# Optimization experiments

Measured on AMD Instinct MI355X. Metric: run time of the kernel, lower is better.

## Reference

```python
import jax, jax.numpy as jnp
import numpy as np

# Fixed problem sizes (equal-sized batch segments, matching setup_inputs)
B, N, M = 4, 4096, 16384          # clouds, coarse pts/cloud, fine pts/cloud
C_IN, C_SKIP, K = 256, 256, 3     # feature dims, knn k
CH = [C_IN + C_SKIP, 512, 256]    # MLP channels
EPS = 1e-16


def setup_inputs() -> dict:
    key = jax.random.key(0)
    ks = jax.random.split(key, 6)
    x = jax.random.normal(ks[0], (B * N, C_IN), jnp.float32)
    pos = jax.random.uniform(ks[1], (B * N, 3), jnp.float32)
    batch = jnp.repeat(jnp.arange(B, dtype=jnp.int64), N)
    x_skip = jax.random.normal(ks[2], (B * M, C_SKIP), jnp.float32)
    pos_skip = jax.random.uniform(ks[3], (B * M, 3), jnp.float32)
    batch_skip = jnp.repeat(jnp.arange(B, dtype=jnp.int64), M)
    W1 = jax.random.normal(ks[4], (CH[0], CH[1]), jnp.float32) / np.sqrt(CH[0]).astype(np.float32)
    b1 = jnp.zeros((CH[1],), jnp.float32)
    W2 = jax.random.normal(ks[5], (CH[1], CH[2]), jnp.float32) / np.sqrt(CH[1]).astype(np.float32)
    b2 = jnp.zeros((CH[2],), jnp.float32)
    return dict(x=x, pos=pos, batch=batch, x_skip=x_skip, pos_skip=pos_skip,
                batch_skip=batch_skip, W1=W1, b1=b1, W2=W2, b2=b2)


def _knn_interpolate(x, pos, pos_skip):
    """torch_geometric.nn.knn_interpolate with equal-sized batch segments."""
    xb = x.reshape(B, N, C_IN)
    ps = pos.reshape(B, N, 3)
    qs = pos_skip.reshape(B, M, 3)
    # squared pairwise distances [B, M, N]
    d2 = (jnp.sum(qs * qs, -1)[:, :, None]
          - 2.0 * jnp.einsum('bmd,bnd->bmn', qs, ps)
          + jnp.sum(ps * ps, -1)[:, None, :])
    neg_d2, idx = jax.lax.top_k(-d2, K)                # k smallest distances, [B,M,K]
    w = 1.0 / jnp.clip(-neg_d2, EPS)                   # inverse squared distance weights
    feats = jax.vmap(lambda f, i: f[i])(xb, idx)       # gather: [B, M, K, C_IN]
    y = jnp.sum(w[..., None] * feats, axis=2) / jnp.sum(w, axis=2)[..., None]
    return y.reshape(B * M, C_IN)


def reference(x, pos, batch, x_skip, pos_skip, batch_skip, W1, b1, W2, b2):
    y = _knn_interpolate(x, pos, pos_skip)
    h = jnp.concatenate([y, x_skip], axis=1)           # [B*M, 512]
    h = jax.nn.relu(h @ W1 + b1)
    h = jax.nn.relu(h @ W2 + b2)
    return h, pos_skip, batch_skip
```

## Files before the change

### kernel.cpp

```cpp
#include <hip/hip_runtime.h>
#include <stdint.h>

#define NB 4
#define NPTS 4096
#define MPTS 16384
#define CIN 256
#define CH0 512
#define CH1 512
#define CH2 256
#define ROWS (NB * MPTS)
#define POS_OUT_OFF (ROWS * CH2)
#define BATCH_OUT_OFF (POS_OUT_OFF + ROWS * 3)
#define CELL_CAP 40
#define QCAP 96

using u16 = unsigned short;
using u32 = unsigned int;
using u64 = unsigned long long;

typedef __bf16 bf16x8 __attribute__((ext_vector_type(8)));
typedef float f32x4 __attribute__((ext_vector_type(4)));

__device__ __forceinline__ u16 f2bf(float f) {
  u32 u = __builtin_bit_cast(u32, f);
  u32 r = u + 0x7fffu + ((u >> 16) & 1u);
  return (u16)(r >> 16);
}

__device__ __forceinline__ u32 flipf(float f) {
  u32 u = __builtin_bit_cast(u32, f);
  return u ^ ((u32)((int)u >> 31) | 0x80000000u);
}
__device__ __forceinline__ float unflipf(u32 f) {
  u32 m = (~(u32)((int)f >> 31)) | 0x80000000u;
  return __builtin_bit_cast(float, f ^ m);
}

__device__ __forceinline__ void ins3(u64 v, u64& k0, u64& k1, u64& k2) {
  u64 a = k0 < v ? v : k0;
  k0 = k0 < v ? k0 : v;
  u64 bb = k1 < a ? a : k1;
  k1 = k1 < a ? k1 : a;
  k2 = k2 < bb ? k2 : bb;
}

__device__ __forceinline__ void merge3(u64 r0, u64 r1, u64 r2,
                                       u64& k0, u64& k1, u64& k2) {
  u64 t = k0 < r0 ? r0 : k0;
  k0 = k0 < r0 ? k0 : r0;
  u64 u = k1 < r1 ? k1 : r1;
  u64 mtu = t < u ? u : t;
  k1 = t < u ? t : u;
  u64 v = k2 < r2 ? k2 : r2;
  k2 = mtu < v ? mtu : v;
}

__device__ __forceinline__ u64 shfl_xor_u64_w8(u64 v, int mask) {
  u32 lo = (u32)v, hi = (u32)(v >> 32);
  lo = (u32)__shfl_xor((int)lo, mask, 8);
  hi = (u32)__shfl_xor((int)hi, mask, 8);
  return ((u64)hi << 32) | lo;
}

__global__ __launch_bounds__(256) void prep_kernel(
    const float* __restrict__ W1, const float* __restrict__ W2,
    u16* __restrict__ W1s, u16* __restrict__ W2s) {
  const int t = blockIdx.x * 256 + threadIdx.x;
  if (t < 32768) {
    const int l = t & 63, ni = (t >> 6) & 3, wd = (t >> 8) & 7, kt = t >> 11;
    const int fr = l & 15, g = l >> 4;
    const int n = wd * 64 + ni * 16 + fr;
    u16 o[8];
#pragma unroll
    for (int j = 0; j < 8; ++j)
      o[j] = f2bf(W1[(kt * 32 + g * 8 + j) * CH1 + n]);
    *(uint4*)(W1s + (size_t)t * 8) = *(const uint4*)o;
  } else {
    const int c = t - 32768;
    const int l = c & 63, ni = (c >> 6) & 1, wd = (c >> 7) & 7, kt = c >> 10;
    const int fr = l & 15, g = l >> 4;
    const int n = wd * 32 + ni * 16 + fr;
    u16 o[8];
#pragma unroll
    for (int j = 0; j < 8; ++j)
      o[j] = f2bf(W2[(kt * 32 + g * 8 + j) * CH2 + n]);
    *(uint4*)(W2s + (size_t)c * 8) = *(const uint4*)o;
  }
}

__global__ __launch_bounds__(256) void tail_kernel(
    const float* __restrict__ pos_skip, const int* __restrict__ batch_skip,
    float* __restrict__ out) {
  int t = blockIdx.x * 256 + threadIdx.x;
  if (t < ROWS * 3) {
    out[POS_OUT_OFF + t] = pos_skip[t];
  } else {
    int u = t - ROWS * 3;
    out[BATCH_OUT_OFF + u] = (float)batch_skip[u];
  }
}

__global__ __launch_bounds__(256) void build_kernel(
    const float* __restrict__ pos, float4* __restrict__ pts4,
    u32* __restrict__ cellCnt, int* __restrict__ cellIdx) {
#pragma clang fp contract(off)
  const int i = blockIdx.x * 256 + threadIdx.x;
  const float x = pos[i * 3 + 0], y = pos[i * 3 + 1], z = pos[i * 3 + 2];
  pts4[i] = make_float4(x, y, z, (x * x + y * y) + z * z);
  const int b = i >> 12;
  int cx = (int)(x * 8.0f); cx = cx < 0 ? 0 : (cx > 7 ? 7 : cx);
  int cy = (int)(y * 8.0f); cy = cy < 0 ? 0 : (cy > 7 ? 7 : cy);
  int cz = (int)(z * 8.0f); cz = cz < 0 ? 0 : (cz > 7 ? 7 : cz);
  const int c = b * 512 + cz * 64 + cy * 8 + cx;
  const u32 slot = atomicAdd(&cellCnt[c], 1u);
  if (slot < CELL_CAP) cellIdx[c * CELL_CAP + slot] = i;
}

__global__ __launch_bounds__(256) void qbin_kernel(
    const float* __restrict__ pos_skip, u32* __restrict__ qCnt,
    int* __restrict__ qIdx) {
  const int q = blockIdx.x * 256 + threadIdx.x;
  const int b = q >> 14;
  const float qx = pos_skip[q * 3 + 0];
  const float qy = pos_skip[q * 3 + 1];
  const float qz = pos_skip[q * 3 + 2];
  int cx = (int)(qx * 8.0f); cx = cx < 0 ? 0 : (cx > 7 ? 7 : cx);
  int cy = (int)(qy * 8.0f); cy = cy < 0 ? 0 : (cy > 7 ? 7 : cy);
  int cz = (int)(qz * 8.0f); cz = cz < 0 ? 0 : (cz > 7 ? 7 : cz);
  const int c = b * 512 + cz * 64 + cy * 8 + cx;
  const u32 slot = atomicAdd(&qCnt[c], 1u);
  if (slot < QCAP) qIdx[c * QCAP + slot] = q;
}

__global__ __launch_bounds__(256) void knn_kernel(
    const float4* __restrict__ pts4, const u32* __restrict__ cellCnt,
    const int* __restrict__ cellIdx, const u32* __restrict__ qCnt,
    const int* __restrict__ qIdx, const float* __restrict__ pos_skip,
    int* __restrict__ idx_out, float* __restrict__ w_out) {
#pragma clang fp contract(off)
  __shared__ float4 scand[27 * CELL_CAP];
  __shared__ int    scgi[27 * CELL_CAP];
  __shared__ u32    scnt[27];
  __shared__ int    sbase[27];
  __shared__ u32    nCand;
  const int tid = threadIdx.x;
  const int b = blockIdx.x >> 9;
  const int cell = blockIdx.x & 511;
  const int cz = cell >> 6, cy = (cell >> 3) & 7, cx = cell & 7;
  const int x0 = cx > 0 ? cx - 1 : 0, x1 = cx < 7 ? cx + 1 : 7;
  const int y0 = cy > 0 ? cy - 1 : 0, y1 = cy < 7 ? cy + 1 : 7;
  const int z0 = cz > 0 ? cz - 1 : 0, z1 = cz < 7 ? cz + 1 : 7;
  const int nx = x1 - x0 + 1, ny = y1 - y0 + 1, nz = z1 - z0 + 1;
  const int ncells = nx * ny * nz;
  if (tid == 0) nCand = 0;
  if (tid < ncells) {
    const int lz = tid / (nx * ny);
    const int rem = tid - lz * nx * ny;
    const int ly = rem / nx;
    const int lx = rem - ly * nx;
    const int cg = b * 512 + (z0 + lz) * 64 + (y0 + ly) * 8 + (x0 + lx);
    u32 cnt = cellCnt[cg];
    scnt[tid] = cnt > CELL_CAP ? CELL_CAP : cnt;
    sbase[tid] = cg * CELL_CAP;
  }
  __syncthreads();
  const int slots = ncells * CELL_CAP;
  for (int s = tid; s < slots; s += 256) {
    const int ci = s / CELL_CAP;
    const int sl = s - ci * CELL_CAP;
    if ((u32)sl < scnt[ci]) {
      const int gi = cellIdx[sbase[ci] + sl];
      const float4 p = pts4[gi];
      const u32 d = atomicAdd(&nCand, 1u);
      scand[d] = p;
      scgi[d] = gi;
    }
  }
  __syncthreads();
  const int nC = (int)nCand;
  u32 nq = qCnt[b * 512 + cell];
  if (nq > QCAP) nq = QCAP;
  const int qbase = (b * 512 + cell) * QCAP;
  const int g = tid >> 3;
  const int sub = tid & 7;

  for (int r0q = 0; r0q < (int)nq; r0q += 32) {
    const int qslot = r0q + g;
    if (qslot < (int)nq) {
      const int q = qIdx[qbase + qslot];
      const float qx = pos_skip[q * 3 + 0];
      const float qy = pos_skip[q * 3 + 1];
      const float qz = pos_skip[q * 3 + 2];
      const float q2 = (qx * qx + qy * qy) + qz * qz;
      u64 k0 = ~0ull, k1 = ~0ull, k2 = ~0ull;
      for (int s = sub; s < nC; s += 8) {
        const float4 p = scand[s];
        const float dot = fmaf(qz, p.z, fmaf(qy, p.y, qx * p.x));
        const float tv = (q2 - 2.0f * dot) + p.w;
        const u64 key = ((u64)flipf(tv) << 32) | (u32)scgi[s];
        ins3(key, k0, k1, k2);
      }
#pragma unroll
      for (int mask = 1; mask < 8; mask <<= 1) {
        const u64 r0 = shfl_xor_u64_w8(k0, mask);
        const u64 r1 = shfl_xor_u64_w8(k1, mask);
        const u64 r2 = shfl_xor_u64_w8(k2, mask);
        merge3(r0, r1, r2, k0, k1, k2);
      }
      float m2tv = unflipf((u32)(k2 >> 32));
      if (!(m2tv <= 0.015625f - 1e-5f)) {
        k0 = k1 = k2 = ~0ull;
        const int ex0 = cx > 1 ? cx - 2 : 0, ex1 = cx < 6 ? cx + 2 : 7;
        const int ey0 = cy > 1 ? cy - 2 : 0, ey1 = cy < 6 ? cy + 2 : 7;
        const int ez0 = cz > 1 ? cz - 2 : 0, ez1 = cz < 6 ? cz + 2 : 7;
        for (int zz = ez0; zz <= ez1; ++zz)
          for (int yy = ey0; yy <= ey1; ++yy)
            for (int xx = ex0; xx <= ex1; ++xx) {
              const int cg = b * 512 + zz * 64 + yy * 8 + xx;
              u32 cnt = cellCnt[cg];
              if (cnt > CELL_CAP) cnt = CELL_CAP;
              const int cb = cg * CELL_CAP;
              for (int s = sub; s < (int)cnt; s += 8) {
                const int gi = cellIdx[cb + s];
                const float4 p = pts4[gi];
                const float dot = fmaf(qz, p.z, fmaf(qy, p.y, qx * p.x));
                const float tv = (q2 - 2.0f * dot) + p.w;
                ins3(((u64)flipf(tv) << 32) | (u32)gi, k0, k1, k2);
              }
            }
#pragma unroll
        for (int mask = 1; mask < 8; mask <<= 1) {
          const u64 r0 = shfl_xor_u64_w8(k0, mask);
          const u64 r1 = shfl_xor_u64_w8(k1, mask);
          const u64 r2 = shfl_xor_u64_w8(k2, mask);
          merge3(r0, r1, r2, k0, k1, k2);
        }
        m2tv = unflipf((u32)(k2 >> 32));
        if (!(m2tv <= 0.0625f - 1e-5f)) {
          k0 = k1 = k2 = ~0ull;
          const int base = b * NPTS;
          for (int i = sub; i < NPTS; i += 8) {
            const int gi = base + i;
            const float4 p = pts4[gi];
            const float dot = fmaf(qz, p.z, fmaf(qy, p.y, qx * p.x));
            const float tv = (q2 - 2.0f * dot) + p.w;
            ins3(((u64)flipf(tv) << 32) | (u32)gi, k0, k1, k2);
          }
#pragma unroll
          for (int mask = 1; mask < 8; mask <<= 1) {
            const u64 r0 = shfl_xor_u64_w8(k0, mask);
            const u64 r1 = shfl_xor_u64_w8(k1, mask);
            const u64 r2 = shfl_xor_u64_w8(k2, mask);
            merge3(r0, r1, r2, k0, k1, k2);
          }
        }
      }
      if (sub == 0) {
        const float t0 = unflipf((u32)(k0 >> 32));
        const float t1 = unflipf((u32)(k1 >> 32));
        const float t2 = unflipf((u32)(k2 >> 32));
        const float w0 = 1.0f / fmaxf(t0, 1e-16f);
        const float w1 = 1.0f / fmaxf(t1, 1e-16f);
        const float w2 = 1.0f / fmaxf(t2, 1e-16f);
        const float wsum = (w0 + w1) + w2;
        const float inv = 1.0f / wsum;
        idx_out[q * 3 + 0] = (int)(u32)k0;
        idx_out[q * 3 + 1] = (int)(u32)k1;
        idx_out[q * 3 + 2] = (int)(u32)k2;
        w_out[q * 3 + 0] = w0 * inv;
        w_out[q * 3 + 1] = w1 * inv;
        w_out[q * 3 + 2] = w2 * inv;
      }
    }
  }
}

__global__ __launch_bounds__(512, 2) void fused_mlp_kernel(
    const float* __restrict__ x, const int* __restrict__ idx,
    const float* __restrict__ w, const float* __restrict__ x_skip,
    const u16* __restrict__ W1s, const float* __restrict__ b1,
    const u16* __restrict__ W2s, const float* __restrict__ b2,
    float* __restrict__ out) {
  __shared__ __align__(16) u16 Abuf[64 * 512];
  const int tid = threadIdx.x;
  const int m0 = blockIdx.x * 64;

  {
    const int row = tid >> 3;
    const int sub = tid & 7;
    const int gr = m0 + row;
    u16* rowp = Abuf + row * 512;
    const int rx = row & 7;
    if (sub < 4) {
      const int i0 = idx[gr * 3 + 0], i1 = idx[gr * 3 + 1], i2 = idx[gr * 3 + 2];
      const float w0 = w[gr * 3 + 0], w1 = w[gr * 3 + 1], w2 = w[gr * 3 + 2];
      const float4* p0 = (const float4*)(x + (size_t)i0 * CIN + sub * 64);
      const float4* p1 = (const float4*)(x + (size_t)i1 * CIN + sub * 64);
      const float4* p2 = (const float4*)(x + (size_t)i2 * CIN + sub * 64);
#pragma unroll
      for (int c = 0; c < 8; ++c) {
        const float4 a0 = p0[c * 2], a1 = p1[c * 2], a2 = p2[c * 2];
        const float4 d0 = p0[c * 2 + 1], d1 = p1[c * 2 + 1], d2 = p2[c * 2 + 1];
        u16 o[8];
        o[0] = f2bf(fmaf(w0, a0.x, fmaf(w1, a1.x, w2 * a2.x)));
        o[1] = f2bf(fmaf(w0, a0.y, fmaf(w1, a1.y, w2 * a2.y)));
        o[2] = f2bf(fmaf(w0, a0.z, fmaf(w1, a1.z, w2 * a2.z)));
        o[3] = f2bf(fmaf(w0, a0.w, fmaf(w1, a1.w, w2 * a2.w)));
        o[4] = f2bf(fmaf(w0, d0.x, fmaf(w1, d1.x, w2 * d2.x)));
        o[5] = f2bf(fmaf(w0, d0.y, fmaf(w1, d1.y, w2 * d2.y)));
        o[6] = f2bf(fmaf(w0, d0.z, fmaf(w1, d1.z, w2 * d2.z)));
        o[7] = f2bf(fmaf(w0, d0.w, fmaf(w1, d1.w, w2 * d2.w)));
        const int vg = sub * 8 + c;
        *(uint4*)(rowp + (vg ^ rx) * 8) = *(const uint4*)o;
      }
    } else {
      const float4* ps = (const float4*)(x_skip + (size_t)gr * CIN + (sub - 4) * 64);
#pragma unroll
      for (int c = 0; c < 8; ++c) {
        const float4 a = ps[c * 2], d = ps[c * 2 + 1];
        u16 o[8];
        o[0] = f2bf(a.x); o[1] = f2bf(a.y); o[2] = f2bf(a.z); o[3] = f2bf(a.w);
        o[4] = f2bf(d.x); o[5] = f2bf(d.y); o[6] = f2bf(d.z); o[7] = f2bf(d.w);
        const int vg = 32 + (sub - 4) * 8 + c;
        *(uint4*)(rowp + (vg ^ rx) * 8) = *(const uint4*)o;
      }
    }
  }
  __syncthreads();

  const int wid = tid >> 6;
  const int lane = tid & 63;
  const int fr = lane & 15;
  const int g = lane >> 4;
  const int frx = fr & 7;

  f32x4 acc[4][4];
#pragma unroll
  for (int mi = 0; mi < 4; mi++)
#pragma unroll
    for (int ni = 0; ni < 4; ni++) acc[mi][ni] = (f32x4){0.f, 0.f, 0.f, 0.f};

  {
    const u16* B1 = W1s + wid * 2048 + lane * 8;
    bf16x8 bf[2][4];
#pragma unroll
    for (int ni = 0; ni < 4; ni++)
      bf[0][ni] = *(const bf16x8*)(B1 + ni * 512);
    for (int kt = 0; kt < 16; ++kt) {
      const int cur = kt & 1;
      if (kt < 15) {
        const u16* nb = B1 + (kt + 1) * 16384;
#pragma unroll
        for (int ni = 0; ni < 4; ni++)
          bf[cur ^ 1][ni] = *(const bf16x8*)(nb + ni * 512);
      }
      bf16x8 af[4];
#pragma unroll
      for (int mi = 0; mi < 4; mi++)
        af[mi] = *(const bf16x8*)&Abuf[(mi * 16 + fr) * 512 +
                                       (((kt * 4 + g) ^ frx) * 8)];
#pragma unroll
      for (int mi = 0; mi < 4; mi++)
#pragma unroll
        for (int ni = 0; ni < 4; ni++)
          acc[mi][ni] = __builtin_amdgcn_mfma_f32_16x16x32_bf16(
              af[mi], bf[cur][ni], acc[mi][ni], 0, 0, 0);
    }
  }
  __syncthreads();

  {
    const int wn = wid * 64;
#pragma unroll
    for (int ni = 0; ni < 4; ni++) {
      const int n = wn + ni * 16 + fr;
      const float bb = b1[n];
      const int vg = n >> 3;
      const int nlow = n & 7;
#pragma unroll
      for (int mi = 0; mi < 4; mi++) {
#pragma unroll
        for (int r = 0; r < 4; r++) {
          const int m = mi * 16 + g * 4 + r;
          const float v = fmaxf(acc[mi][ni][r] + bb, 0.f);
          Abuf[m * 512 + (vg ^ (m & 7)) * 8 + nlow] = f2bf(v);
        }
      }
    }
  }
  __syncthreads();

  f32x4 acc2[4][2];
#pragma unroll
  for (int mi = 0; mi < 4; mi++)
#pragma unroll
    for (int ni = 0; ni < 2; ni++) acc2[mi][ni] = (f32x4){0.f, 0.f, 0.f, 0.f};

  {
    const u16* B2 = W2s + wid * 1024 + lane * 8;
    bf16x8 bf[2][2];
#pragma unroll
    for (int ni = 0; ni < 2; ni++)
      bf[0][ni] = *(const bf16x8*)(B2 + ni * 512);
    for (int kt = 0; kt < 16; ++kt) {
      const int cur = kt & 1;
      if (kt < 15) {
        const u16* nb = B2 + (kt + 1) * 8192;
#pragma unroll
        for (int ni = 0; ni < 2; ni++)
          bf[cur ^ 1][ni] = *(const bf16x8*)(nb + ni * 512);
      }
      bf16x8 af[4];
#pragma unroll
      for (int mi = 0; mi < 4; mi++)
        af[mi] = *(const bf16x8*)&Abuf[(mi * 16 + fr) * 512 +
                                       (((kt * 4 + g) ^ frx) * 8)];
#pragma unroll
      for (int mi = 0; mi < 4; mi++)
#pragma unroll
        for (int ni = 0; ni < 2; ni++)
          acc2[mi][ni] = __builtin_amdgcn_mfma_f32_16x16x32_bf16(
              af[mi], bf[cur][ni], acc2[mi][ni], 0, 0, 0);
    }
  }

#pragma unroll
  for (int ni = 0; ni < 2; ni++) {
    const int col = wid * 32 + ni * 16 + fr;
    const float bb = b2[col];
#pragma unroll
    for (int mi = 0; mi < 4; mi++) {
#pragma unroll
      for (int r = 0; r < 4; r++) {
        const int rowg = m0 + mi * 16 + g * 4 + r;
        out[(size_t)rowg * CH2 + col] = fmaxf(acc2[mi][ni][r] + bb, 0.f);
      }
    }
  }
}

extern "C" void kernel_launch(void* const* d_in, const int* in_sizes, int n_in,
                              void* d_out, int out_size, void* d_ws, size_t ws_size,
                              hipStream_t stream) {
  const float* x        = (const float*)d_in[0];
  const float* pos      = (const float*)d_in[1];
  const float* x_skip   = (const float*)d_in[3];
  const float* pos_skip = (const float*)d_in[4];
  const int*   batch_sk = (const int*)d_in[5];
  const float* W1       = (const float*)d_in[6];
  const float* b1       = (const float*)d_in[7];
  const float* W2       = (const float*)d_in[8];
  const float* b2       = (const float*)d_in[9];
  float* out = (float*)d_out;

  char* ws = (char*)d_ws;
  u16*    W1s     = (u16*)(ws);
  u16*    W2s     = (u16*)(ws + 524288);
  int*    idxb    = (int*)(ws + 786432);
  float*  wb      = (float*)(ws + 1572864);
  float4* pts4    = (float4*)(ws + 2359296);
  u32*    cellCnt = (u32*)(ws + 2621440);
  u32*    qCnt    = (u32*)(ws + 2629632);
  int*    cellIdx = (int*)(ws + 2637824);
  int*    qIdx    = (int*)(ws + 2965504);

  hipMemsetAsync(cellCnt, 0, 16384, stream);
  prep_kernel<<<dim3(192), dim3(256), 0, stream>>>(W1, W2, W1s, W2s);
  tail_kernel<<<dim3(1024), dim3(256), 0, stream>>>(pos_skip, batch_sk, out);
  build_kernel<<<dim3(64), dim3(256), 0, stream>>>(pos, pts4, cellCnt, cellIdx);
  qbin_kernel<<<dim3(256), dim3(256), 0, stream>>>(pos_skip, qCnt, qIdx);
  knn_kernel<<<dim3(2048), dim3(256), 0, stream>>>(pts4, cellCnt, cellIdx,
                                                   qCnt, qIdx, pos_skip,
                                                   idxb, wb);
  fused_mlp_kernel<<<dim3(1024), dim3(512), 0, stream>>>(
      x, idxb, wb, x_skip, W1s, b1, W2s, b2, out);
}
```

Before: 264.1 us.

## Merge small prep kernels and rebalance the gather so every thread loads interpolated and skip features

Fuses prep+tail into one launch and build+qbin into another, cutting the launch count by two. In the MLP, each of the 8 threads per row now handles a 32-column slice of both the interpolated and the skip features, instead of half the threads doing the 3-way gather and half copying skip. The LDS swizzle is changed to match, and the A-fragment reads and layer-1 writeback are updated accordingly. This balances load work across threads, at the cost of more live registers during the gather.

```diff
diff --git a/kernel.cpp b/kernel.cpp
--- a/kernel.cpp
+++ b/kernel.cpp
@@ -62,74 +62,75 @@
   return ((u64)hi << 32) | lo;
 }
 
-__global__ __launch_bounds__(256) void prep_kernel(
+__global__ __launch_bounds__(256) void preptail_kernel(
     const float* __restrict__ W1, const float* __restrict__ W2,
-    u16* __restrict__ W1s, u16* __restrict__ W2s) {
-  const int t = blockIdx.x * 256 + threadIdx.x;
-  if (t < 32768) {
-    const int l = t & 63, ni = (t >> 6) & 3, wd = (t >> 8) & 7, kt = t >> 11;
-    const int fr = l & 15, g = l >> 4;
-    const int n = wd * 64 + ni * 16 + fr;
-    u16 o[8];
-#pragma unroll
-    for (int j = 0; j < 8; ++j)
-      o[j] = f2bf(W1[(kt * 32 + g * 8 + j) * CH1 + n]);
-    *(uint4*)(W1s + (size_t)t * 8) = *(const uint4*)o;
-  } else {
-    const int c = t - 32768;
-    const int l = c & 63, ni = (c >> 6) & 1, wd = (c >> 7) & 7, kt = c >> 10;
-    const int fr = l & 15, g = l >> 4;
-    const int n = wd * 32 + ni * 16 + fr;
-    u16 o[8];
-#pragma unroll
-    for (int j = 0; j < 8; ++j)
-      o[j] = f2bf(W2[(kt * 32 + g * 8 + j) * CH2 + n]);
-    *(uint4*)(W2s + (size_t)c * 8) = *(const uint4*)o;
-  }
-}
-
-__global__ __launch_bounds__(256) void tail_kernel(
+    u16* __restrict__ W1s, u16* __restrict__ W2s,
     const float* __restrict__ pos_skip, const int* __restrict__ batch_skip,
     float* __restrict__ out) {
-  int t = blockIdx.x * 256 + threadIdx.x;
-  if (t < ROWS * 3) {
-    out[POS_OUT_OFF + t] = pos_skip[t];
+  const int bid = blockIdx.x;
+  if (bid < 192) {
+    const int t = bid * 256 + threadIdx.x;
+    if (t < 32768) {
+      const int l = t & 63, ni = (t >> 6) & 3, wd = (t >> 8) & 7, kt = t >> 11;
+      const int fr = l & 15, g = l >> 4;
+      const int n = wd * 64 + ni * 16 + fr;
+      u16 o[8];
+#pragma unroll
+      for (int j = 0; j < 8; ++j)
+        o[j] = f2bf(W1[(kt * 32 + g * 8 + j) * CH1 + n]);
+      *(uint4*)(W1s + (size_t)t * 8) = *(const uint4*)o;
+    } else {
+      const int c = t - 32768;
+      const int l = c & 63, ni = (c >> 6) & 1, wd = (c >> 7) & 7, kt = c >> 10;
+      const int fr = l & 15, g = l >> 4;
+      const int n = wd * 32 + ni * 16 + fr;
+      u16 o[8];
+#pragma unroll
+      for (int j = 0; j < 8; ++j)
+        o[j] = f2bf(W2[(kt * 32 + g * 8 + j) * CH2 + n]);
+      *(uint4*)(W2s + (size_t)c * 8) = *(const uint4*)o;
+    }
   } else {
-    int u = t - ROWS * 3;
-    out[BATCH_OUT_OFF + u] = (float)batch_skip[u];
-  }
-}
-
-__global__ __launch_bounds__(256) void build_kernel(
+    const int t = (bid - 192) * 256 + threadIdx.x;
+    if (t < ROWS * 3) {
+      out[POS_OUT_OFF + t] = pos_skip[t];
+    } else {
+      int u = t - ROWS * 3;
+      out[BATCH_OUT_OFF + u] = (float)batch_skip[u];
+    }
+  }
+}
+
+__global__ __launch_bounds__(256) void bin_kernel(
     const float* __restrict__ pos, float4* __restrict__ pts4,
-    u32* __restrict__ cellCnt, int* __restrict__ cellIdx) {
-#pragma clang fp contract(off)
-  const int i = blockIdx.x * 256 + threadIdx.x;
-  const float x = pos[i * 3 + 0], y = pos[i * 3 + 1], z = pos[i * 3 + 2];
-  pts4[i] = make_float4(x, y, z, (x * x + y * y) + z * z);
-  const int b = i >> 12;
-  int cx = (int)(x * 8.0f); cx = cx < 0 ? 0 : (cx > 7 ? 7 : cx);
-  int cy = (int)(y * 8.0f); cy = cy < 0 ? 0 : (cy > 7 ? 7 : cy);
-  int cz = (int)(z * 8.0f); cz = cz < 0 ? 0 : (cz > 7 ? 7 : cz);
-  const int c = b * 512 + cz * 64 + cy * 8 + cx;
-  const u32 slot = atomicAdd(&cellCnt[c], 1u);
-  if (slot < CELL_CAP) cellIdx[c * CELL_CAP + slot] = i;
-}
-
-__global__ __launch_bounds__(256) void qbin_kernel(
+    u32* __restrict__ cellCnt, int* __restrict__ cellIdx,
     const float* __restrict__ pos_skip, u32* __restrict__ qCnt,
     int* __restrict__ qIdx) {
-  const int q = blockIdx.x * 256 + threadIdx.x;
-  const int b = q >> 14;
-  const float qx = pos_skip[q * 3 + 0];
-  const float qy = pos_skip[q * 3 + 1];
-  const float qz = pos_skip[q * 3 + 2];
-  int cx = (int)(qx * 8.0f); cx = cx < 0 ? 0 : (cx > 7 ? 7 : cx);
-  int cy = (int)(qy * 8.0f); cy = cy < 0 ? 0 : (cy > 7 ? 7 : cy);
-  int cz = (int)(qz * 8.0f); cz = cz < 0 ? 0 : (cz > 7 ? 7 : cz);
-  const int c = b * 512 + cz * 64 + cy * 8 + cx;
-  const u32 slot = atomicAdd(&qCnt[c], 1u);
-  if (slot < QCAP) qIdx[c * QCAP + slot] = q;
+#pragma clang fp contract(off)
+  if (blockIdx.x < 64) {
+    const int i = blockIdx.x * 256 + threadIdx.x;
+    const float x = pos[i * 3 + 0], y = pos[i * 3 + 1], z = pos[i * 3 + 2];
+    pts4[i] = make_float4(x, y, z, (x * x + y * y) + z * z);
+    const int b = i >> 12;
+    int cx = (int)(x * 8.0f); cx = cx < 0 ? 0 : (cx > 7 ? 7 : cx);
+    int cy = (int)(y * 8.0f); cy = cy < 0 ? 0 : (cy > 7 ? 7 : cy);
+    int cz = (int)(z * 8.0f); cz = cz < 0 ? 0 : (cz > 7 ? 7 : cz);
+    const int c = b * 512 + cz * 64 + cy * 8 + cx;
+    const u32 slot = atomicAdd(&cellCnt[c], 1u);
+    if (slot < CELL_CAP) cellIdx[c * CELL_CAP + slot] = i;
+  } else {
+    const int q = (blockIdx.x - 64) * 256 + threadIdx.x;
+    const int b = q >> 14;
+    const float qx = pos_skip[q * 3 + 0];
+    const float qy = pos_skip[q * 3 + 1];
+    const float qz = pos_skip[q * 3 + 2];
+    int cx = (int)(qx * 8.0f); cx = cx < 0 ? 0 : (cx > 7 ? 7 : cx);
+    int cy = (int)(qy * 8.0f); cy = cy < 0 ? 0 : (cy > 7 ? 7 : cy);
+    int cz = (int)(qz * 8.0f); cz = cz < 0 ? 0 : (cz > 7 ? 7 : cz);
+    const int c = b * 512 + cz * 64 + cy * 8 + cx;
+    const u32 slot = atomicAdd(&qCnt[c], 1u);
+    if (slot < QCAP) qIdx[c * QCAP + slot] = q;
+  }
 }
 
 __global__ __launch_bounds__(256) void knn_kernel(
@@ -291,39 +292,44 @@
     const int gr = m0 + row;
     u16* rowp = Abuf + row * 512;
     const int rx = row & 7;
-    if (sub < 4) {
-      const int i0 = idx[gr * 3 + 0], i1 = idx[gr * 3 + 1], i2 = idx[gr * 3 + 2];
-      const float w0 = w[gr * 3 + 0], w1 = w[gr * 3 + 1], w2 = w[gr * 3 + 2];
-      const float4* p0 = (const float4*)(x + (size_t)i0 * CIN + sub * 64);
-      const float4* p1 = (const float4*)(x + (size_t)i1 * CIN + sub * 64);
-      const float4* p2 = (const float4*)(x + (size_t)i2 * CIN + sub * 64);
-#pragma unroll
-      for (int c = 0; c < 8; ++c) {
-        const float4 a0 = p0[c * 2], a1 = p1[c * 2], a2 = p2[c * 2];
-        const float4 d0 = p0[c * 2 + 1], d1 = p1[c * 2 + 1], d2 = p2[c * 2 + 1];
-        u16 o[8];
-        o[0] = f2bf(fmaf(w0, a0.x, fmaf(w1, a1.x, w2 * a2.x)));
-        o[1] = f2bf(fmaf(w0, a0.y, fmaf(w1, a1.y, w2 * a2.y)));
-        o[2] = f2bf(fmaf(w0, a0.z, fmaf(w1, a1.z, w2 * a2.z)));
-        o[3] = f2bf(fmaf(w0, a0.w, fmaf(w1, a1.w, w2 * a2.w)));
-        o[4] = f2bf(fmaf(w0, d0.x, fmaf(w1, d1.x, w2 * d2.x)));
-        o[5] = f2bf(fmaf(w0, d0.y, fmaf(w1, d1.y, w2 * d2.y)));
-        o[6] = f2bf(fmaf(w0, d0.z, fmaf(w1, d1.z, w2 * d2.z)));
-        o[7] = f2bf(fmaf(w0, d0.w, fmaf(w1, d1.w, w2 * d2.w)));
-        const int vg = sub * 8 + c;
-        *(uint4*)(rowp + (vg ^ rx) * 8) = *(const uint4*)o;
-      }
-    } else {
-      const float4* ps = (const float4*)(x_skip + (size_t)gr * CIN + (sub - 4) * 64);
-#pragma unroll
-      for (int c = 0; c < 8; ++c) {
-        const float4 a = ps[c * 2], d = ps[c * 2 + 1];
-        u16 o[8];
-        o[0] = f2bf(a.x); o[1] = f2bf(a.y); o[2] = f2bf(a.z); o[3] = f2bf(a.w);
-        o[4] = f2bf(d.x); o[5] = f2bf(d.y); o[6] = f2bf(d.z); o[7] = f2bf(d.w);
-        const int vg = 32 + (sub - 4) * 8 + c;
-        *(uint4*)(rowp + (vg ^ rx) * 8) = *(const uint4*)o;
-      }
+    const float4* ps = (const float4*)(x_skip + (size_t)gr * CIN + sub * 32);
+    float4 sv0 = ps[0], sv1 = ps[1], sv2 = ps[2], sv3 = ps[3];
+    float4 sv4 = ps[4], sv5 = ps[5], sv6 = ps[6], sv7 = ps[7];
+    const int i0 = idx[gr * 3 + 0], i1 = idx[gr * 3 + 1], i2 = idx[gr * 3 + 2];
+    const float w0 = w[gr * 3 + 0], w1 = w[gr * 3 + 1], w2 = w[gr * 3 + 2];
+    const float4* p0 = (const float4*)(x + (size_t)i0 * CIN + sub * 32);
+    const float4* p1 = (const float4*)(x + (size_t)i1 * CIN + sub * 32);
+    const float4* p2 = (const float4*)(x + (size_t)i2 * CIN + sub * 32);
+#pragma unroll
+    for (int c = 0; c < 4; ++c) {
+      const float4 a0 = p0[c * 2], a1 = p1[c * 2], a2 = p2[c * 2];
+      const float4 d0 = p0[c * 2 + 1], d1 = p1[c * 2 + 1], d2 = p2[c * 2 + 1];
+      u16 o[8];
+      o[0] = f2bf(fmaf(w0, a0.x, fmaf(w1, a1.x, w2 * a2.x)));
+      o[1] = f2bf(fmaf(w0, a0.y, fmaf(w1, a1.y, w2 * a2.y)));
+      o[2] = f2bf(fmaf(w0, a0.z, fmaf(w1, a1.z, w2 * a2.z)));
+      o[3] = f2bf(fmaf(w0, a0.w, fmaf(w1, a1.w, w2 * a2.w)));
+      o[4] = f2bf(fmaf(w0, d0.x, fmaf(w1, d1.x, w2 * d2.x)));
+      o[5] = f2bf(fmaf(w0, d0.y, fmaf(w1, d1.y, w2 * d2.y)));
+      o[6] = f2bf(fmaf(w0, d0.z, fmaf(w1, d1.z, w2 * d2.z)));
+      o[7] = f2bf(fmaf(w0, d0.w, fmaf(w1, d1.w, w2 * d2.w)));
+      const int p = (c << 3) | (sub ^ rx);
+      *(uint4*)(rowp + p * 8) = *(const uint4*)o;
+    }
+    {
+      u16 o[8];
+      o[0]=f2bf(sv0.x); o[1]=f2bf(sv0.y); o[2]=f2bf(sv0.z); o[3]=f2bf(sv0.w);
+      o[4]=f2bf(sv1.x); o[5]=f2bf(sv1.y); o[6]=f2bf(sv1.z); o[7]=f2bf(sv1.w);
+      *(uint4*)(rowp + (32 | (0 << 3) | (sub ^ rx)) * 8) = *(const uint4*)o;
+      o[0]=f2bf(sv2.x); o[1]=f2bf(sv2.y); o[2]=f2bf(sv2.z); o[3]=f2bf(sv2.w);
+      o[4]=f2bf(sv3.x); o[5]=f2bf(sv3.y); o[6]=f2bf(sv3.z); o[7]=f2bf(sv3.w);
+      *(uint4*)(rowp + (32 | (1 << 3) | (sub ^ rx)) * 8) = *(const uint4*)o;
+      o[0]=f2bf(sv4.x); o[1]=f2bf(sv4.y); o[2]=f2bf(sv4.z); o[3]=f2bf(sv4.w);
+      o[4]=f2bf(sv5.x); o[5]=f2bf(sv5.y); o[6]=f2bf(sv5.z); o[7]=f2bf(sv5.w);
+      *(uint4*)(rowp + (32 | (2 << 3) | (sub ^ rx)) * 8) = *(const uint4*)o;
+      o[0]=f2bf(sv6.x); o[1]=f2bf(sv6.y); o[2]=f2bf(sv6.z); o[3]=f2bf(sv6.w);
+      o[4]=f2bf(sv7.x); o[5]=f2bf(sv7.y); o[6]=f2bf(sv7.z); o[7]=f2bf(sv7.w);
+      *(uint4*)(rowp + (32 | (3 << 3) | (sub ^ rx)) * 8) = *(const uint4*)o;
     }
   }
   __syncthreads();
@@ -358,7 +364,7 @@
 #pragma unroll
       for (int mi = 0; mi < 4; mi++)
         af[mi] = *(const bf16x8*)&Abuf[(mi * 16 + fr) * 512 +
-                                       (((kt * 4 + g) ^ frx) * 8)];
+            ((((kt >> 3) << 5) | (g << 3) | ((kt & 7) ^ frx)) * 8)];
 #pragma unroll
       for (int mi = 0; mi < 4; mi++)
 #pragma unroll
@@ -377,13 +383,14 @@
       const float bb = b1[n];
       const int vg = n >> 3;
       const int nlow = n & 7;
+      const int pb = (vg & 32) | ((vg & 3) << 3) | ((vg >> 2) & 7);
 #pragma unroll
       for (int mi = 0; mi < 4; mi++) {
 #pragma unroll
         for (int r = 0; r < 4; r++) {
           const int m = mi * 16 + g * 4 + r;
           const float v = fmaxf(acc[mi][ni][r] + bb, 0.f);
-          Abuf[m * 512 + (vg ^ (m & 7)) * 8 + nlow] = f2bf(v);
+          Abuf[m * 512 + (pb ^ (m & 7)) * 8 + nlow] = f2bf(v);
         }
       }
     }
@@ -414,7 +421,7 @@
 #pragma unroll
       for (int mi = 0; mi < 4; mi++)
         af[mi] = *(const bf16x8*)&Abuf[(mi * 16 + fr) * 512 +
-                                       (((kt * 4 + g) ^ frx) * 8)];
+            ((((kt >> 3) << 5) | (g << 3) | ((kt & 7) ^ frx)) * 8)];
 #pragma unroll
       for (int mi = 0; mi < 4; mi++)
 #pragma unroll
@@ -465,10 +472,10 @@
   int*    qIdx    = (int*)(ws + 2965504);
 
   hipMemsetAsync(cellCnt, 0, 16384, stream);
-  prep_kernel<<<dim3(192), dim3(256), 0, stream>>>(W1, W2, W1s, W2s);
-  tail_kernel<<<dim3(1024), dim3(256), 0, stream>>>(pos_skip, batch_sk, out);
-  build_kernel<<<dim3(64), dim3(256), 0, stream>>>(pos, pts4, cellCnt, cellIdx);
-  qbin_kernel<<<dim3(256), dim3(256), 0, stream>>>(pos_skip, qCnt, qIdx);
+  preptail_kernel<<<dim3(1216), dim3(256), 0, stream>>>(
+      W1, W2, W1s, W2s, pos_skip, batch_sk, out);
+  bin_kernel<<<dim3(320), dim3(256), 0, stream>>>(
+      pos, pts4, cellCnt, cellIdx, pos_skip, qCnt, qIdx);
   knn_kernel<<<dim3(2048), dim3(256), 0, stream>>>(pts4, cellCnt, cellIdx,
                                                    qCnt, qIdx, pos_skip,
                                                    idxb, wb);
```

New measurement: 270.0 us. 2.2% more time.
